# Optimization experiments

Measured on AMD Instinct MI355X. Metric: run time of the kernel, lower is better.

## Reference

```python
import jax, jax.numpy as jnp
import numpy as np
from functools import partial

# --- constants from module init / yolov5 NMS conventions ---
CONF_THRES = 0.25
IOU_THRES = 0.45
PATCH_CONF = 0.001
GN = jnp.array([640.0, 640.0, 640.0, 640.0])  # img_size[[1,0,1,0]]
MAX_WH = 4096.0       # per-class NMS offset trick
K_CLEAN = 256         # fixed-size cap for clean detections (max_det=1000 effectively)
K_PATCH = 1024        # fixed-size cap for patch detections (max_det=30000 effectively)
MAXDET_CLEAN = 1000
MAXDET_PATCH = 30000
B, N, NC = 8, 25200, 80


def xywh2xyxy(x):
    xy, wh = x[..., :2], x[..., 2:4]
    return jnp.concatenate([xy - wh * 0.5, xy + wh * 0.5], axis=-1)


def pairwise_iou(a, b):
    # a: [A,4], b: [B,4] -> [A,B] jaccard overlap (same math as IoU.get_iou)
    tl = jnp.maximum(a[:, None, :2], b[None, :, :2])
    br = jnp.minimum(a[:, None, 2:], b[None, :, 2:])
    wh = jnp.clip(br - tl, 0.0)
    inter = wh[..., 0] * wh[..., 1]
    area_a = (a[:, 2] - a[:, 0]) * (a[:, 3] - a[:, 1])
    area_b = (b[:, 2] - b[:, 0]) * (b[:, 3] - b[:, 1])
    return inter / (area_a[:, None] + area_b[None, :] - inter)


def greedy_nms(iou_mat, valid, iou_thres):
    # iou_mat: [K,K] (score-sorted order), valid: [K] bool. Greedy suppression.
    K = valid.shape[0]
    j = jnp.arange(K)

    def body(i, keep):
        suppress = keep[i] & (iou_mat[i] > iou_thres) & (j > i)
        return keep & ~suppress

    return jax.lax.fori_loop(0, K, body, valid)


def _nms_single(pred, conf_thres, K, max_det):
    # pred: [N, 5+nc] raw yolov5 prediction for one image
    boxes = xywh2xyxy(pred[:, :4])
    obj = pred[:, 4]
    cls_scores = pred[:, 5:] * obj[:, None]          # conf = obj * cls
    conf = cls_scores.max(axis=-1)
    cls = jnp.argmax(cls_scores, axis=-1).astype(pred.dtype)
    valid = (obj > conf_thres) & (conf > conf_thres)
    mscore = jnp.where(valid, conf, -1.0)
    _, idx = jax.lax.top_k(mscore, K)                # fixed-size candidate prefilter
    bk, ck, vk = boxes[idx], cls[idx], valid[idx]
    off_boxes = bk + (ck * MAX_WH)[:, None]          # class-offset NMS
    iou = pairwise_iou(off_boxes, off_boxes)
    keep = greedy_nms(jax.lax.stop_gradient(iou), vk, IOU_THRES)
    keep = keep & (jnp.cumsum(keep.astype(jnp.int32)) <= max_det)
    return bk, ck, keep


def _forward(output_clean, output_patch):
    nms_clean = jax.vmap(lambda p: _nms_single(p, CONF_THRES, K_CLEAN, MAXDET_CLEAN))
    nms_patch = jax.vmap(lambda p: _nms_single(p, PATCH_CONF, K_PATCH, MAXDET_PATCH))
    bc, cc, kc = nms_clean(output_clean)   # [B,Kc,4],[B,Kc],[B,Kc]
    bp, cp, kp = nms_patch(output_patch)   # [B,Kp,4],[B,Kp],[B,Kp]
    bc_n = bc / GN
    bp_n = bp / GN

    def per_img(bp_i, cp_i, kp_i, bc_i, cc_i, kc_i):
        iou = pairwise_iou(bp_i, bc_i)                       # [Kp, Kc]
        match = kp_i[:, None] & (cp_i[:, None] == cc_i[None, :])
        tm = jnp.max(jnp.where(match, iou, 0.0), axis=0)     # max IoU per clean det
        return jnp.sum(jnp.where(kc_i, tm, 0.0)), jnp.sum(kc_i.astype(jnp.float32))

    sums, counts = jax.vmap(per_img)(bp_n, cp, kp, bc_n, cc, kc)
    total, cnt = sums.sum(), counts.sum()
    return jnp.where(cnt > 0, 1.0 - total / jnp.maximum(cnt, 1.0), 1.0)


def setup_inputs() -> dict:
    key = jax.random.key(0)
    k1, k2 = jax.random.split(key)

    def make(k):
        kxy, kwh, ko, kc = jax.random.split(k, 4)
        xy = jax.random.uniform(kxy, (B, N, 2)) * 608.0 + 16.0   # centers in-frame
        wh = jax.random.uniform(kwh, (B, N, 2)) * 96.0 + 8.0     # plausible box sizes
        obj = jax.random.uniform(ko, (B, N, 1))
        cls = jax.random.uniform(kc, (B, N, NC))
        return jnp.concatenate([xy, wh, obj, cls], axis=-1)

    return {"output_clean": make(k1), "output_patch": make(k2)}


def reference(output_clean, output_patch):
    return _forward(output_clean, output_patch)
```

## Files before the change

kernel.cpp:

```cpp
#include <hip/hip_runtime.h>

#define N_ANCH 25200
#define NCLS   80
#define ROW    85
#define NIMG   16
#define KMAX   1024
#define NBINS  4096
#define CAND_CAP 4096
#define SC2_RPC 16
#define SC2_CPI 1575
#define SC2_CHUNKS (NIMG * SC2_CPI)
#define SC2_CFLOATS (SC2_RPC * ROW)
#define SC2_BLOCKS 1792
#define PCHUNK 64
#define CCNT_STRIDE 16

typedef unsigned long long u64;
typedef unsigned int u32;

#define OFF_KEYS 0ull
#define OFF_HIST 3225600ull
#define OFF_TBIN 3487744ull
#define OFF_CCNT 3487808ull
#define OFF_SUMS 3488832ull
#define OFF_CNTS 3488864ull
#define OFF_CAND 3488896ull
#define OFF_SEL  4013184ull
#define OFF_BOX  4144256ull
#define OFF_CLS  4406400ull
#define OFF_RINIT 4471936ull
#define OFF_KEEP 4473984ull
#define WS_NEED  4539520ull
#define ZERO_BYTES (262144ull + 64 + 1024 + 32 + 32)

#define DMA16(gsrc, ldst) \
    __builtin_amdgcn_global_load_lds( \
        (const __attribute__((address_space(1))) void*)(gsrc), \
        (__attribute__((address_space(3))) void*)(ldst), 16, 0, 0)

__device__ __forceinline__ int key_bin(u64 key) {
    u32 hi = (u32)(key >> 32);
    if (hi == 0u) return 0;
    float conf = __uint_as_float(hi - 0x40000000u);
    int b = 1 + (int)(conf * 4093.0f);
    return b > 4094 ? 4094 : b;
}

__device__ __forceinline__ u64 readlane64(u64 v, int src) {
    u32 lo = (u32)__builtin_amdgcn_readlane((int)(u32)(v & 0xffffffffull), src);
    u32 hi = (u32)__builtin_amdgcn_readlane((int)(u32)(v >> 32), src);
    return ((u64)hi << 32) | (u64)lo;
}

__device__ __forceinline__ u64 shfl64_xor(u64 v, int m) {
    int lo = __shfl_xor((int)(u32)(v & 0xffffffffull), m, 64);
    int hi = __shfl_xor((int)(u32)(v >> 32), m, 64);
    return ((u64)(u32)hi << 32) | (u64)(u32)lo;
}

__device__ __forceinline__ void sc_issue(const float* __restrict__ clean,
                                         const float* __restrict__ patch,
                                         int c, int lane, float* buf)
{
    const int b = c / SC2_CPI;
    const int ch = c - b * SC2_CPI;
    const float* g = ((b < 8) ? clean + (size_t)b * N_ANCH * ROW
                              : patch + (size_t)(b - 8) * N_ANCH * ROW)
                     + (size_t)ch * SC2_CFLOATS;
    #pragma unroll
    for (int u = 0; u < 5; ++u)
        DMA16(g + u * 256 + lane * 4, buf + u * 256);
    if (lane < 20)
        DMA16(g + 5 * 256 + lane * 4, buf + 5 * 256);
}

__device__ __forceinline__ void sc_compute(int c, int lane,
                                           const float* buf, u64* __restrict__ keys)
{
    const int b = c / SC2_CPI;
    const int ch = c - b * SC2_CPI;
    const int r = lane & 15, h = lane >> 4;
    const float* p = buf + r * ROW;
    const float obj = p[4];
    float best = -1.0f; int bc = 0;
    #pragma unroll
    for (int d = 0; d < 20; ++d) {
        const float s = p[5 + h * 20 + d] * obj;
        if (s > best) { best = s; bc = h * 20 + d; }
    }
    #pragma unroll
    for (int m = 16; m <= 32; m <<= 1) {
        const float o = __shfl_xor(best, m, 64);
        const int  oc = __shfl_xor(bc, m, 64);
        if (o > best || (o == best && oc < bc)) { best = o; bc = oc; }
    }
    if (h == 0) {
        const int n = ch * SC2_RPC + r;
        const float th = (b < 8) ? 0.25f : 0.001f;
        const bool valid = (obj > th) && (best > th);
        const u32 hi = valid ? (__float_as_uint(best) + 0x40000000u) : 0u;
        const u32 nbar = 32767u - (u32)n;
        keys[(size_t)b * N_ANCH + n] =
            ((u64)hi << 32) | ((u64)nbar << 8) | (u64)(u32)bc;
    }
}

__global__ __launch_bounds__(128) void k_score(const float* __restrict__ clean,
                                               const float* __restrict__ patch,
                                               u64* __restrict__ keys)
{
    __shared__ float lds[2][2][SC2_CFLOATS];
    const int wv = threadIdx.x >> 6, lane = threadIdx.x & 63;
    const int wid = blockIdx.x * 2 + wv;
    const int stride = SC2_BLOCKS * 2;
    int cur = 0;
    sc_issue(clean, patch, wid, lane, &lds[wv][0][0]);
    for (int c = wid; c < SC2_CHUNKS; c += stride) {
        const int cn = c + stride;
        if (cn < SC2_CHUNKS) {
            sc_issue(clean, patch, cn, lane, &lds[wv][cur ^ 1][0]);
            asm volatile("s_waitcnt vmcnt(6)" ::: "memory");
        } else {
            asm volatile("s_waitcnt vmcnt(0)" ::: "memory");
        }
        __builtin_amdgcn_sched_barrier(0);
        sc_compute(c, lane, &lds[wv][cur][0], keys);
        cur ^= 1;
    }
}

__global__ __launch_bounds__(256) void k_hist(const u64* __restrict__ keys,
                                              int* __restrict__ hist)
{
    __shared__ int h[NBINS];
    const int b = blockIdx.x;
    for (int i = threadIdx.x; i < NBINS; i += 256) h[i] = 0;
    __syncthreads();
    const int start = blockIdx.y * 1575;
    const u64* kp = keys + (size_t)b * N_ANCH;
    for (int i = start + threadIdx.x; i < start + 1575; i += 256)
        atomicAdd(&h[key_bin(kp[i])], 1);
    __syncthreads();
    for (int i = threadIdx.x; i < NBINS; i += 256)
        if (h[i]) atomicAdd(&hist[b * NBINS + i], h[i]);
}

__global__ __launch_bounds__(1024) void k_thresh(const int* __restrict__ hist,
                                                 int* __restrict__ tbin)
{
    __shared__ int arr[1024];
    const int b = blockIdx.x;
    const int t = threadIdx.x;
    int hh[4];
    hh[0] = hist[b * NBINS + 4 * t + 0];
    hh[1] = hist[b * NBINS + 4 * t + 1];
    hh[2] = hist[b * NBINS + 4 * t + 2];
    hh[3] = hist[b * NBINS + 4 * t + 3];
    const int r = hh[0] + hh[1] + hh[2] + hh[3];
    arr[t] = r;
    __syncthreads();
    for (int off = 1; off < 1024; off <<= 1) {
        int v = (t + off < 1024) ? arr[t + off] : 0;
        __syncthreads();
        arr[t] += v;
        __syncthreads();
    }
    const int K = (b < 8) ? 256 : 1024;
    int cb = arr[t] - r;
    for (int d = 3; d >= 0; --d) {
        int ca = cb + hh[d];
        if (cb < K && ca >= K) tbin[b] = 4 * t + d;
        cb = ca;
    }
}

__global__ __launch_bounds__(256) void k_compact(const u64* __restrict__ keys,
                                                 const int* __restrict__ tbin,
                                                 int* __restrict__ ccnt,
                                                 u64* __restrict__ cand)
{
    const int b = blockIdx.x;
    const int T = tbin[b];
    const u64* kp = keys + (size_t)b * N_ANCH;
    const int start = blockIdx.y * 1575;
    const int lane = threadIdx.x & 63;
    #pragma unroll
    for (int it = 0; it < 7; ++it) {
        const int off = it * 256 + threadIdx.x;
        const bool in = off < 1575;
        const u64 key = in ? kp[start + off] : 0ull;
        const bool cnd = in && (key_bin(key) >= T);
        const u64 bal = __ballot(cnd);
        if (bal) {
            int base = 0;
            if (lane == 0) base = atomicAdd(&ccnt[b * CCNT_STRIDE], __popcll(bal));
            base = __shfl(base, 0, 64);
            if (cnd) {
                const int pos = base + __popcll(bal & ((1ull << lane) - 1ull));
                if (pos < CAND_CAP) cand[(size_t)b * CAND_CAP + pos] = key;
            }
        }
    }
}

__global__ __launch_bounds__(1024) void k_sort(const u64* __restrict__ cand,
                                               const int* __restrict__ ccnt,
                                               u64* __restrict__ sel)
{
    __shared__ u64 sk[CAND_CAP];
    const int b = blockIdx.x;
    const int C = min(ccnt[b * CCNT_STRIDE], CAND_CAP);
    const int t = threadIdx.x;
    u64 e0, e1, e2, e3;
    e0 = (t < C) ? cand[(size_t)b * CAND_CAP + t] : 0ull;
    e1 = (1024 + t < C) ? cand[(size_t)b * CAND_CAP + 1024 + t] : 0ull;
    e2 = (2048 + t < C) ? cand[(size_t)b * CAND_CAP + 2048 + t] : 0ull;
    e3 = (3072 + t < C) ? cand[(size_t)b * CAND_CAP + 3072 + t] : 0ull;

    #define CSWAP_D(a, c) { if ((a) < (c)) { u64 _t = (a); (a) = (c); (c) = _t; } }
    #define CSWAP_A(a, c) { if ((a) > (c)) { u64 _t = (a); (a) = (c); (c) = _t; } }

    for (int k = 2; k <= 4096; k <<= 1) {
        for (int j = k >> 1; j > 0; j >>= 1) {
            if (j >= 1024) {
                if (j == 2048) {
                    CSWAP_D(e0, e2); CSWAP_D(e1, e3);
                } else {
                    if (k == 4096) { CSWAP_D(e0, e1); CSWAP_D(e2, e3); }
                    else           { CSWAP_D(e0, e1); CSWAP_A(e2, e3); }
                }
            } else if (j >= 64) {
                __syncthreads();
                sk[t] = e0; sk[1024 + t] = e1; sk[2048 + t] = e2; sk[3072 + t] = e3;
                __syncthreads();
                const int tp = t ^ j;
                #pragma unroll
                for (int p = 0; p < 4; ++p) {
                    const int i = p * 1024 + t;
                    const u64 cv = (p == 0) ? e0 : (p == 1) ? e1 : (p == 2) ? e2 : e3;
                    const u64 o = sk[p * 1024 + tp];
                    const bool take_max = (((i & k) == 0) == ((t & j) == 0));
                    const u64 mx = cv > o ? cv : o;
                    const u64 mn = cv > o ? o : cv;
                    const u64 nv = take_max ? mx : mn;
                    if (p == 0) e0 = nv; else if (p == 1) e1 = nv;
                    else if (p == 2) e2 = nv; else e3 = nv;
                }
            } else {
                #pragma unroll
                for (int p = 0; p < 4; ++p) {
                    const int i = p * 1024 + t;
                    const u64 cv = (p == 0) ? e0 : (p == 1) ? e1 : (p == 2) ? e2 : e3;
                    const u64 o = shfl64_xor(cv, j);
                    const bool take_max = (((i & k) == 0) == ((t & j) == 0));
                    const u64 mx = cv > o ? cv : o;
                    const u64 mn = cv > o ? o : cv;
                    const u64 nv = take_max ? mx : mn;
                    if (p == 0) e0 = nv; else if (p == 1) e1 = nv;
                    else if (p == 2) e2 = nv; else e3 = nv;
                }
            }
        }
    }
    const int K = (b < 8) ? 256 : 1024;
    if (t < K) sel[b * KMAX + t] = e0;
    #undef CSWAP_D
    #undef CSWAP_A
}

__global__ __launch_bounds__(1024) void k_gather(const float* __restrict__ clean,
                                                 const float* __restrict__ patch,
                                                 const u64* __restrict__ sel,
                                                 float4* __restrict__ boxes,
                                                 int* __restrict__ cls,
                                                 u64* __restrict__ rinit)
{
    const int b = blockIdx.x;
    const int t = threadIdx.x;
    const int K = (b < 8) ? 256 : 1024;
    const u64 key = (t < K) ? sel[b * KMAX + t] : 0ull;
    const u32 hi = (u32)(key >> 32);
    const bool valid = (t < K) && (hi != 0u);
    u64 bal = __ballot(valid);
    if ((t & 63) == 0) rinit[b * 16 + (t >> 6)] = ~bal;
    if (t >= K) return;
    const int n = 32767 - (int)((key >> 8) & 0x7FFFu);
    const int c = (int)(key & 0x7Fu);
    const float* src = ((b < 8) ? (clean + (size_t)b * N_ANCH * ROW)
                                : (patch + (size_t)(b - 8) * N_ANCH * ROW)) + (size_t)n * ROW;
    const float x = src[0], y = src[1], w = src[2], h = src[3];
    boxes[b * KMAX + t] = make_float4(x - w * 0.5f, y - h * 0.5f, x + w * 0.5f, y + h * 0.5f);
    cls[b * KMAX + t] = c;
}

__global__ __launch_bounds__(1024) void k_nms_mask(const float4* __restrict__ boxes,
                                                   const int* __restrict__ cls,
                                                   u64* __restrict__ mask,
                                                   u64* __restrict__ diag)
{
    __shared__ float4 bx[KMAX];
    __shared__ float ar[KMAX];
    const int b = blockIdx.x;
    const int K = (b < 8) ? 256 : 1024;
    const int row0 = blockIdx.y * 64;
    if (row0 >= K) return;
    const int t = threadIdx.x;
    for (int i = t; i < K; i += 1024) {
        float4 v = boxes[b * KMAX + i];
        float off = (float)cls[b * KMAX + i] * 4096.0f;
        v.x += off; v.y += off; v.z += off; v.w += off;
        bx[i] = v;
        ar[i] = (v.z - v.x) * (v.w - v.y);
    }
    __syncthreads();
    const int w   = t >> 6;
    const int row = row0 + (t & 63);
    u64* dst = mask + ((size_t)b * KMAX + row) * 16 + w;
    if (((w << 6) + 63) <= row0 && row0 > 0) { *dst = 0ull; return; }
    const float4 bi = bx[row];
    const float ai = ar[row];
    const int jbase = w << 6;
    u64 m = 0;
    #pragma unroll 8
    for (int k = 0; k < 64; ++k) {
        const int j = jbase + k;
        const float4 bj = bx[j];
        const float ax = fmaxf(bi.x, bj.x), ay = fmaxf(bi.y, bj.y);
        const float bx2 = fminf(bi.z, bj.z), by2 = fminf(bi.w, bj.w);
        const float iw = fmaxf(bx2 - ax, 0.f), ih = fmaxf(by2 - ay, 0.f);
        const float inter = iw * ih;
        const float iou = inter / (ai + ar[j] - inter);
        if (j > row && iou > 0.45f) m |= (1ull << k);
    }
    *dst = m;
    if (w == (row0 >> 6)) diag[(size_t)b * KMAX + row] = m;
}

__global__ __launch_bounds__(1024) void k_nms_scan(const u64* __restrict__ mask,
                                                   const u64* __restrict__ diag,
                                                   const u64* __restrict__ rinit,
                                                   int* __restrict__ keep)
{
    extern __shared__ u64 smem[];
    const int b = blockIdx.x;
    const int K = (b < 8) ? 256 : 1024;
    const int W = K >> 6;
    const int t = threadIdx.x;
    u64* smask = smem;
    u64* sdiag = smem + (size_t)K * 16;
    {
        const float4* s4 = (const float4*)(mask + (size_t)b * KMAX * 16);
        float4* d4 = (float4*)smask;
        const int n4 = (K * 16) >> 1;
        for (int i = t; i < n4; i += 1024) d4[i] = s4[i];
        const float4* s4d = (const float4*)(diag + (size_t)b * KMAX);
        float4* d4d = (float4*)sdiag;
        for (int i = t; i < (K >> 1); i += 1024) d4d[i] = s4d[i];
    }
    __syncthreads();
    if (t >= 64) return;
    const int lane = t;
    const int q = lane >> 4;
    const int wl = lane & 15;
    u64 w_remv = rinit[b * 16 + wl];
    u64 ow = readlane64(w_remv, 0);
    u64 dj = sdiag[lane];
    for (int g = 0; g < W; ++g) {
        u64 nz = __ballot(dj != 0ull);
        u64 o = ow;
        while (nz) {
            const int j = (int)__builtin_ctzll(nz);
            nz &= nz - 1;
            if (!((o >> j) & 1ull)) o |= readlane64(dj, j);
        }
        const u64 kept = ~o;
        if (g + 1 < W) dj = sdiag[(g + 1) * 64 + lane];
        const u64* mrow = smask + (size_t)(g * 64 + q * 16) * 16 + wl;
        const u32 kg = (u32)((kept >> (q * 16)) & 0xFFFFull);
        u64 a0 = 0, a1 = 0;
        #pragma unroll
        for (int i = 0; i < 16; i += 2) {
            const u64 m0 = mrow[(size_t)(i + 0) * 16];
            const u64 m1 = mrow[(size_t)(i + 1) * 16];
            a0 |= ((kg >> i) & 1u) ? m0 : 0ull;
            a1 |= ((kg >> (i + 1)) & 1u) ? m1 : 0ull;
        }
        u64 part = a0 | a1;
        part |= shfl64_xor(part, 16);
        part |= shfl64_xor(part, 32);
        w_remv |= part;
        if (g + 1 < W) ow = readlane64(w_remv, g + 1);
    }
    if (lane < W) {
        #pragma unroll
        for (int k = 0; k < 64; ++k)
            keep[b * KMAX + lane * 64 + k] = (int)(((w_remv >> k) & 1) ^ 1ull);
    }
}

__global__ __launch_bounds__(256) void k_match_partial(const float4* __restrict__ boxes,
                                                       const int* __restrict__ cls,
                                                       const int* __restrict__ keep,
                                                       float* __restrict__ pmax)
{
    __shared__ float4 pb[PCHUNK];
    __shared__ float par[PCHUNK];
    __shared__ int pcls[PCHUNK];
    const int c = blockIdx.x;
    const int p = blockIdx.y;
    const int bp = 8 + c;
    const int t = threadIdx.x;
    if (t < PCHUNK) {
        const int i = p * PCHUNK + t;
        const float4 v = boxes[bp * KMAX + i];
        pb[t] = v;
        par[t] = (v.z - v.x) * (v.w - v.y);
        pcls[t] = keep[bp * KMAX + i] ? cls[bp * KMAX + i] : -1;
    }
    __syncthreads();
    const float4 bc = boxes[c * KMAX + t];
    const int cc = cls[c * KMAX + t];
    const float area_c = (bc.z - bc.x) * (bc.w - bc.y);
    float tm = 0.f;
    #pragma unroll 8
    for (int i = 0; i < PCHUNK; ++i) {
        const float4 bi = pb[i];
        const float ax = fmaxf(bi.x, bc.x), ay = fmaxf(bi.y, bc.y);
        const float bx2 = fminf(bi.z, bc.z), by2 = fminf(bi.w, bc.w);
        const float iw = fmaxf(bx2 - ax, 0.f), ih = fmaxf(by2 - ay, 0.f);
        const float inter = iw * ih;
        const float iou = inter / (par[i] + area_c - inter);
        tm = fmaxf(tm, (pcls[i] == cc) ? iou : 0.f);
    }
    pmax[(c * 16 + p) * 256 + t] = tm;
}

__global__ __launch_bounds__(256) void k_match_reduce(const float* __restrict__ pmax,
                                                      const int* __restrict__ keep,
                                                      float* __restrict__ sums,
                                                      float* __restrict__ cnts)
{
    __shared__ float red[8];
    const int c = blockIdx.x;
    const int t = threadIdx.x;
    float tm = 0.f;
    #pragma unroll
    for (int p = 0; p < 16; ++p)
        tm = fmaxf(tm, pmax[(c * 16 + p) * 256 + t]);
    const int kc = keep[c * KMAX + t];
    float val = kc ? tm : 0.f;
    float cv  = kc ? 1.f : 0.f;
    for (int off = 32; off > 0; off >>= 1) {
        val += __shfl_down(val, off);
        cv  += __shfl_down(cv, off);
    }
    const int wv = t >> 6, lane = t & 63;
    if (lane == 0) { red[wv] = val; red[4 + wv] = cv; }
    __syncthreads();
    if (t == 0) {
        sums[c] = red[0] + red[1] + red[2] + red[3];
        cnts[c] = red[4] + red[5] + red[6] + red[7];
    }
}

__global__ void k_final(const float* __restrict__ sums,
                        const float* __restrict__ cnts,
                        float* __restrict__ out)
{
    if (threadIdx.x == 0 && blockIdx.x == 0) {
        float total = 0.f, cnt = 0.f;
        for (int c = 0; c < 8; ++c) { total += sums[c]; cnt += cnts[c]; }
        out[0] = (cnt > 0.f) ? (1.0f - total / fmaxf(cnt, 1.0f)) : 1.0f;
    }
}

extern "C" void kernel_launch(void* const* d_in, const int* in_sizes, int n_in,
                              void* d_out, int out_size, void* d_ws, size_t ws_size,
                              hipStream_t stream)
{
    if (ws_size < WS_NEED) return;
    const float* clean = (const float*)d_in[0];
    const float* patch = (const float*)d_in[1];
    float* out = (float*)d_out;
    char* ws = (char*)d_ws;

    u64*    keys = (u64*)(ws + OFF_KEYS);
    u64*    mask = (u64*)(ws + OFF_KEYS);
    int*    hist = (int*)(ws + OFF_HIST);
    u64*    diag = (u64*)(ws + OFF_HIST);
    int*    tbin = (int*)(ws + OFF_TBIN);
    int*    ccnt = (int*)(ws + OFF_CCNT);
    float*  sums = (float*)(ws + OFF_SUMS);
    float*  cnts = (float*)(ws + OFF_CNTS);
    u64*    cand = (u64*)(ws + OFF_CAND);
    float*  pmax = (float*)(ws + OFF_CAND);
    u64*    sel  = (u64*)(ws + OFF_SEL);
    float4* boxes = (float4*)(ws + OFF_BOX);
    int*    cls  = (int*)(ws + OFF_CLS);
    u64*    rinit = (u64*)(ws + OFF_RINIT);
    int*    keep = (int*)(ws + OFF_KEEP);

    hipMemsetAsync(ws + OFF_HIST, 0, ZERO_BYTES, stream);

    k_score<<<SC2_BLOCKS, 128, 0, stream>>>(clean, patch, keys);
    k_hist<<<dim3(NIMG, 16), 256, 0, stream>>>(keys, hist);
    k_thresh<<<NIMG, 1024, 0, stream>>>(hist, tbin);
    k_compact<<<dim3(NIMG, 16), 256, 0, stream>>>(keys, tbin, ccnt, cand);
    k_sort<<<NIMG, 1024, 0, stream>>>(cand, ccnt, sel);
    k_gather<<<NIMG, 1024, 0, stream>>>(clean, patch, sel, boxes, cls, rinit);
    k_nms_mask<<<dim3(NIMG, 16), 1024, 0, stream>>>(boxes, cls, mask, diag);
    k_nms_scan<<<NIMG, 1024, KMAX * 16 * 8 + KMAX * 8, stream>>>(mask, diag, rinit, keep);
    k_match_partial<<<dim3(8, 16), 256, 0, stream>>>(boxes, cls, keep, pmax);
    k_match_reduce<<<8, 256, 0, stream>>>(pmax, keep, sums, cnts);
    k_final<<<1, 64, 0, stream>>>(sums, cnts, out);
}
```

Baseline: 136.1 us.

## Fuse histogram into scoring, gather into NMS mask, and final reductions

```diff
diff --git a/kernel.cpp b/kernel.cpp
--- a/kernel.cpp
+++ b/kernel.cpp
@@ -5,13 +5,13 @@
 #define ROW    85
 #define NIMG   16
 #define KMAX   1024
-#define NBINS  4096
+#define NBINS  1024
 #define CAND_CAP 4096
 #define SC2_RPC 16
 #define SC2_CPI 1575
-#define SC2_CHUNKS (NIMG * SC2_CPI)
-#define SC2_CFLOATS (SC2_RPC * ROW)
-#define SC2_BLOCKS 1792
+#define SC2_CFLOATS (SC2_RPC*ROW)
+#define SC2_BPI 96
+#define SC2_WPI 192
 #define PCHUNK 64
 #define CCNT_STRIDE 16
 
@@ -20,18 +20,16 @@
 
 #define OFF_KEYS 0ull
 #define OFF_HIST 3225600ull
-#define OFF_TBIN 3487744ull
-#define OFF_CCNT 3487808ull
-#define OFF_SUMS 3488832ull
-#define OFF_CNTS 3488864ull
-#define OFF_CAND 3488896ull
-#define OFF_SEL  4013184ull
-#define OFF_BOX  4144256ull
-#define OFF_CLS  4406400ull
-#define OFF_RINIT 4471936ull
-#define OFF_KEEP 4473984ull
-#define WS_NEED  4539520ull
-#define ZERO_BYTES (262144ull + 64 + 1024 + 32 + 32)
+#define OFF_TBIN 3291136ull
+#define OFF_CCNT 3291200ull
+#define OFF_CAND 3292224ull
+#define OFF_SEL  3816512ull
+#define OFF_BOX  3947584ull
+#define OFF_CLS  4209728ull
+#define OFF_RINIT 4275264ull
+#define OFF_KEEP 4277312ull
+#define WS_NEED  4342848ull
+#define ZERO_BYTES 66624ull
 
 #define DMA16(gsrc, ldst) \
     __builtin_amdgcn_global_load_lds( \
@@ -42,8 +40,8 @@
     u32 hi = (u32)(key >> 32);
     if (hi == 0u) return 0;
     float conf = __uint_as_float(hi - 0x40000000u);
-    int b = 1 + (int)(conf * 4093.0f);
-    return b > 4094 ? 4094 : b;
+    int b = 1 + (int)(conf * 1022.0f);
+    return b > 1023 ? 1023 : b;
 }
 
 __device__ __forceinline__ u64 readlane64(u64 v, int src) {
@@ -58,27 +56,20 @@
     return ((u64)(u32)hi << 32) | (u64)(u32)lo;
 }
 
-__device__ __forceinline__ void sc_issue(const float* __restrict__ clean,
-                                         const float* __restrict__ patch,
-                                         int c, int lane, float* buf)
-{
-    const int b = c / SC2_CPI;
-    const int ch = c - b * SC2_CPI;
-    const float* g = ((b < 8) ? clean + (size_t)b * N_ANCH * ROW
-                              : patch + (size_t)(b - 8) * N_ANCH * ROW)
-                     + (size_t)ch * SC2_CFLOATS;
+__device__ __forceinline__ void sc_issue(const float* __restrict__ img, int ch,
+                                         int lane, float* buf)
+{
+    const float* s = img + (size_t)ch * SC2_CFLOATS;
     #pragma unroll
     for (int u = 0; u < 5; ++u)
-        DMA16(g + u * 256 + lane * 4, buf + u * 256);
+        DMA16(s + u * 256 + lane * 4, buf + u * 256);
     if (lane < 20)
-        DMA16(g + 5 * 256 + lane * 4, buf + 5 * 256);
-}
-
-__device__ __forceinline__ void sc_compute(int c, int lane,
-                                           const float* buf, u64* __restrict__ keys)
-{
-    const int b = c / SC2_CPI;
-    const int ch = c - b * SC2_CPI;
+        DMA16(s + 1280 + lane * 4, buf + 1280);
+}
+
+__device__ __forceinline__ void sc_compute(int b, int c, int lane, const float* buf,
+                                           u64* __restrict__ keys, int* bh)
+{
     const int r = lane & 15, h = lane >> 4;
     const float* p = buf + r * ROW;
     const float obj = p[4];
@@ -95,10 +86,15 @@
         if (o > best || (o == best && oc < bc)) { best = o; bc = oc; }
     }
     if (h == 0) {
-        const int n = ch * SC2_RPC + r;
+        const int n = c * SC2_RPC + r;
         const float th = (b < 8) ? 0.25f : 0.001f;
         const bool valid = (obj > th) && (best > th);
         const u32 hi = valid ? (__float_as_uint(best) + 0x40000000u) : 0u;
+        if (valid) {
+            int bin = 1 + (int)(best * 1022.0f);
+            if (bin > 1023) bin = 1023;
+            atomicAdd(&bh[bin], 1);
+        }
         const u32 nbar = 32767u - (u32)n;
         keys[(size_t)b * N_ANCH + n] =
             ((u64)hi << 32) | ((u64)nbar << 8) | (u64)(u32)bc;
@@ -107,48 +103,43 @@
 
 __global__ __launch_bounds__(128) void k_score(const float* __restrict__ clean,
                                                const float* __restrict__ patch,
-                                               u64* __restrict__ keys)
+                                               u64* __restrict__ keys,
+                                               int* __restrict__ hist)
 {
     __shared__ float lds[2][2][SC2_CFLOATS];
-    const int wv = threadIdx.x >> 6, lane = threadIdx.x & 63;
-    const int wid = blockIdx.x * 2 + wv;
-    const int stride = SC2_BLOCKS * 2;
+    __shared__ int bh[NBINS];
+    const int t = threadIdx.x;
+    const int wv = t >> 6, lane = t & 63;
+    const int b = blockIdx.x / SC2_BPI;
+    const int blk = blockIdx.x - b * SC2_BPI;
+    const int wimg = blk * 2 + wv;
+    for (int i = t; i < NBINS; i += 128) bh[i] = 0;
+    __syncthreads();
+    const float* img = (b < 8) ? clean + (size_t)b * N_ANCH * ROW
+                               : patch + (size_t)(b - 8) * N_ANCH * ROW;
     int cur = 0;
-    sc_issue(clean, patch, wid, lane, &lds[wv][0][0]);
-    for (int c = wid; c < SC2_CHUNKS; c += stride) {
-        const int cn = c + stride;
-        if (cn < SC2_CHUNKS) {
-            sc_issue(clean, patch, cn, lane, &lds[wv][cur ^ 1][0]);
+    sc_issue(img, wimg, lane, &lds[wv][0][0]);
+    for (int c = wimg; c < SC2_CPI; c += SC2_WPI) {
+        const int cn = c + SC2_WPI;
+        if (cn < SC2_CPI) {
+            sc_issue(img, cn, lane, &lds[wv][cur ^ 1][0]);
             asm volatile("s_waitcnt vmcnt(6)" ::: "memory");
         } else {
             asm volatile("s_waitcnt vmcnt(0)" ::: "memory");
         }
         __builtin_amdgcn_sched_barrier(0);
-        sc_compute(c, lane, &lds[wv][cur][0], keys);
+        sc_compute(b, c, lane, &lds[wv][cur][0], keys, bh);
         cur ^= 1;
     }
-}
-
-__global__ __launch_bounds__(256) void k_hist(const u64* __restrict__ keys,
-                                              int* __restrict__ hist)
-{
-    __shared__ int h[NBINS];
-    const int b = blockIdx.x;
-    for (int i = threadIdx.x; i < NBINS; i += 256) h[i] = 0;
-    __syncthreads();
-    const int start = blockIdx.y * 1575;
-    const u64* kp = keys + (size_t)b * N_ANCH;
-    for (int i = start + threadIdx.x; i < start + 1575; i += 256)
-        atomicAdd(&h[key_bin(kp[i])], 1);
-    __syncthreads();
-    for (int i = threadIdx.x; i < NBINS; i += 256)
-        if (h[i]) atomicAdd(&hist[b * NBINS + i], h[i]);
-}
-
-__global__ __launch_bounds__(1024) void k_thresh(const int* __restrict__ hist,
-                                                 int* __restrict__ tbin)
-{
-    __shared__ int arr[1024];
+    __syncthreads();
+    for (int i = t; i < NBINS; i += 128)
+        if (bh[i]) atomicAdd(&hist[b * NBINS + i], bh[i]);
+}
+
+__global__ __launch_bounds__(256) void k_thresh(const int* __restrict__ hist,
+                                                int* __restrict__ tbin)
+{
+    __shared__ int arr[256];
     const int b = blockIdx.x;
     const int t = threadIdx.x;
     int hh[4];
@@ -159,8 +150,8 @@
     const int r = hh[0] + hh[1] + hh[2] + hh[3];
     arr[t] = r;
     __syncthreads();
-    for (int off = 1; off < 1024; off <<= 1) {
-        int v = (t + off < 1024) ? arr[t + off] : 0;
+    for (int off = 1; off < 256; off <<= 1) {
+        int v = (t + off < 256) ? arr[t + off] : 0;
         __syncthreads();
         arr[t] += v;
         __syncthreads();
@@ -216,16 +207,13 @@
     e1 = (1024 + t < C) ? cand[(size_t)b * CAND_CAP + 1024 + t] : 0ull;
     e2 = (2048 + t < C) ? cand[(size_t)b * CAND_CAP + 2048 + t] : 0ull;
     e3 = (3072 + t < C) ? cand[(size_t)b * CAND_CAP + 3072 + t] : 0ull;
-
     #define CSWAP_D(a, c) { if ((a) < (c)) { u64 _t = (a); (a) = (c); (c) = _t; } }
     #define CSWAP_A(a, c) { if ((a) > (c)) { u64 _t = (a); (a) = (c); (c) = _t; } }
-
     for (int k = 2; k <= 4096; k <<= 1) {
         for (int j = k >> 1; j > 0; j >>= 1) {
             if (j >= 1024) {
-                if (j == 2048) {
-                    CSWAP_D(e0, e2); CSWAP_D(e1, e3);
-                } else {
+                if (j == 2048) { CSWAP_D(e0, e2); CSWAP_D(e1, e3); }
+                else {
                     if (k == 4096) { CSWAP_D(e0, e1); CSWAP_D(e2, e3); }
                     else           { CSWAP_D(e0, e1); CSWAP_A(e2, e3); }
                 }
@@ -268,49 +256,44 @@
     #undef CSWAP_A
 }
 
-__global__ __launch_bounds__(1024) void k_gather(const float* __restrict__ clean,
-                                                 const float* __restrict__ patch,
-                                                 const u64* __restrict__ sel,
-                                                 float4* __restrict__ boxes,
-                                                 int* __restrict__ cls,
-                                                 u64* __restrict__ rinit)
-{
-    const int b = blockIdx.x;
-    const int t = threadIdx.x;
-    const int K = (b < 8) ? 256 : 1024;
-    const u64 key = (t < K) ? sel[b * KMAX + t] : 0ull;
-    const u32 hi = (u32)(key >> 32);
-    const bool valid = (t < K) && (hi != 0u);
-    u64 bal = __ballot(valid);
-    if ((t & 63) == 0) rinit[b * 16 + (t >> 6)] = ~bal;
-    if (t >= K) return;
-    const int n = 32767 - (int)((key >> 8) & 0x7FFFu);
-    const int c = (int)(key & 0x7Fu);
-    const float* src = ((b < 8) ? (clean + (size_t)b * N_ANCH * ROW)
-                                : (patch + (size_t)(b - 8) * N_ANCH * ROW)) + (size_t)n * ROW;
-    const float x = src[0], y = src[1], w = src[2], h = src[3];
-    boxes[b * KMAX + t] = make_float4(x - w * 0.5f, y - h * 0.5f, x + w * 0.5f, y + h * 0.5f);
-    cls[b * KMAX + t] = c;
-}
-
-__global__ __launch_bounds__(1024) void k_nms_mask(const float4* __restrict__ boxes,
-                                                   const int* __restrict__ cls,
+__global__ __launch_bounds__(1024) void k_nms_mask(const float* __restrict__ clean,
+                                                   const float* __restrict__ patch,
+                                                   const u64* __restrict__ sel,
+                                                   float4* __restrict__ boxes,
+                                                   int* __restrict__ cls,
+                                                   u64* __restrict__ rinit,
                                                    u64* __restrict__ mask,
                                                    u64* __restrict__ diag)
 {
     __shared__ float4 bx[KMAX];
     __shared__ float ar[KMAX];
-    const int b = blockIdx.x;
+    const int b = blockIdx.x, y = blockIdx.y;
     const int K = (b < 8) ? 256 : 1024;
-    const int row0 = blockIdx.y * 64;
+    const int row0 = y * 64;
     if (row0 >= K) return;
     const int t = threadIdx.x;
-    for (int i = t; i < K; i += 1024) {
-        float4 v = boxes[b * KMAX + i];
-        float off = (float)cls[b * KMAX + i] * 4096.0f;
-        v.x += off; v.y += off; v.z += off; v.w += off;
-        bx[i] = v;
-        ar[i] = (v.z - v.x) * (v.w - v.y);
+    {
+        const u64 key = (t < K) ? sel[b * KMAX + t] : 0ull;
+        const u32 hi = (u32)(key >> 32);
+        const bool valid = (t < K) && (hi != 0u);
+        const u64 bal = __ballot(valid);
+        if (y == 0 && (t & 63) == 0) rinit[b * 16 + (t >> 6)] = ~bal;
+        if (t < K) {
+            const int n = 32767 - (int)((key >> 8) & 0x7FFFu);
+            const int c = (int)(key & 0x7Fu);
+            const float* src = ((b < 8) ? (clean + (size_t)b * N_ANCH * ROW)
+                                        : (patch + (size_t)(b - 8) * N_ANCH * ROW))
+                               + (size_t)n * ROW;
+            const float x = src[0], yy = src[1], w = src[2], h = src[3];
+            const float4 raw = make_float4(x - w * 0.5f, yy - h * 0.5f,
+                                           x + w * 0.5f, yy + h * 0.5f);
+            if (y == 0) { boxes[b * KMAX + t] = raw; cls[b * KMAX + t] = c; }
+            const float off = (float)c * 4096.0f;
+            const float4 ob = make_float4(raw.x + off, raw.y + off,
+                                          raw.z + off, raw.w + off);
+            bx[t] = ob;
+            ar[t] = (ob.z - ob.x) * (ob.w - ob.y);
+        }
     }
     __syncthreads();
     const int w   = t >> 6;
@@ -435,43 +418,36 @@
     pmax[(c * 16 + p) * 256 + t] = tm;
 }
 
-__global__ __launch_bounds__(256) void k_match_reduce(const float* __restrict__ pmax,
-                                                      const int* __restrict__ keep,
-                                                      float* __restrict__ sums,
-                                                      float* __restrict__ cnts)
+__global__ __launch_bounds__(256) void k_match_final(const float* __restrict__ pmax,
+                                                     const int* __restrict__ keep,
+                                                     float* __restrict__ out)
 {
     __shared__ float red[8];
-    const int c = blockIdx.x;
-    const int t = threadIdx.x;
-    float tm = 0.f;
-    #pragma unroll
-    for (int p = 0; p < 16; ++p)
-        tm = fmaxf(tm, pmax[(c * 16 + p) * 256 + t]);
-    const int kc = keep[c * KMAX + t];
-    float val = kc ? tm : 0.f;
-    float cv  = kc ? 1.f : 0.f;
-    for (int off = 32; off > 0; off >>= 1) {
-        val += __shfl_down(val, off);
-        cv  += __shfl_down(cv, off);
-    }
-    const int wv = t >> 6, lane = t & 63;
-    if (lane == 0) { red[wv] = val; red[4 + wv] = cv; }
-    __syncthreads();
-    if (t == 0) {
-        sums[c] = red[0] + red[1] + red[2] + red[3];
-        cnts[c] = red[4] + red[5] + red[6] + red[7];
-    }
-}
-
-__global__ void k_final(const float* __restrict__ sums,
-                        const float* __restrict__ cnts,
-                        float* __restrict__ out)
-{
-    if (threadIdx.x == 0 && blockIdx.x == 0) {
-        float total = 0.f, cnt = 0.f;
-        for (int c = 0; c < 8; ++c) { total += sums[c]; cnt += cnts[c]; }
-        out[0] = (cnt > 0.f) ? (1.0f - total / fmaxf(cnt, 1.0f)) : 1.0f;
-    }
+    const int t = threadIdx.x;
+    float tot = 0.f, cn = 0.f;
+    for (int c = 0; c < 8; ++c) {
+        float tm = 0.f;
+        #pragma unroll
+        for (int p = 0; p < 16; ++p)
+            tm = fmaxf(tm, pmax[(c * 16 + p) * 256 + t]);
+        const int kc = keep[c * KMAX + t];
+        float val = kc ? tm : 0.f;
+        float cv  = kc ? 1.f : 0.f;
+        for (int off = 32; off > 0; off >>= 1) {
+            val += __shfl_down(val, off);
+            cv  += __shfl_down(cv, off);
+        }
+        const int wv = t >> 6, lane = t & 63;
+        if (lane == 0) { red[wv] = val; red[4 + wv] = cv; }
+        __syncthreads();
+        if (t == 0) {
+            tot += red[0] + red[1] + red[2] + red[3];
+            cn  += red[4] + red[5] + red[6] + red[7];
+        }
+        __syncthreads();
+    }
+    if (t == 0)
+        out[0] = (cn > 0.f) ? (1.0f - tot / fmaxf(cn, 1.0f)) : 1.0f;
 }
 
 extern "C" void kernel_launch(void* const* d_in, const int* in_sizes, int n_in,
@@ -487,12 +463,10 @@
     u64*    keys = (u64*)(ws + OFF_KEYS);
     u64*    mask = (u64*)(ws + OFF_KEYS);
     int*    hist = (int*)(ws + OFF_HIST);
-    u64*    diag = (u64*)(ws + OFF_HIST);
     int*    tbin = (int*)(ws + OFF_TBIN);
     int*    ccnt = (int*)(ws + OFF_CCNT);
-    float*  sums = (float*)(ws + OFF_SUMS);
-    float*  cnts = (float*)(ws + OFF_CNTS);
     u64*    cand = (u64*)(ws + OFF_CAND);
+    u64*    diag = (u64*)(ws + OFF_CAND);
     float*  pmax = (float*)(ws + OFF_CAND);
     u64*    sel  = (u64*)(ws + OFF_SEL);
     float4* boxes = (float4*)(ws + OFF_BOX);
@@ -502,15 +476,13 @@
 
     hipMemsetAsync(ws + OFF_HIST, 0, ZERO_BYTES, stream);
 
-    k_score<<<SC2_BLOCKS, 128, 0, stream>>>(clean, patch, keys);
-    k_hist<<<dim3(NIMG, 16), 256, 0, stream>>>(keys, hist);
-    k_thresh<<<NIMG, 1024, 0, stream>>>(hist, tbin);
+    k_score<<<NIMG * SC2_BPI, 128, 0, stream>>>(clean, patch, keys, hist);
+    k_thresh<<<NIMG, 256, 0, stream>>>(hist, tbin);
     k_compact<<<dim3(NIMG, 16), 256, 0, stream>>>(keys, tbin, ccnt, cand);
     k_sort<<<NIMG, 1024, 0, stream>>>(cand, ccnt, sel);
-    k_gather<<<NIMG, 1024, 0, stream>>>(clean, patch, sel, boxes, cls, rinit);
-    k_nms_mask<<<dim3(NIMG, 16), 1024, 0, stream>>>(boxes, cls, mask, diag);
+    k_nms_mask<<<dim3(NIMG, 16), 1024, 0, stream>>>(clean, patch, sel, boxes, cls,
+                                                    rinit, mask, diag);
     k_nms_scan<<<NIMG, 1024, KMAX * 16 * 8 + KMAX * 8, stream>>>(mask, diag, rinit, keep);
     k_match_partial<<<dim3(8, 16), 256, 0, stream>>>(boxes, cls, keep, pmax);
-    k_match_reduce<<<8, 256, 0, stream>>>(pmax, keep, sums, cnts);
-    k_final<<<1, 64, 0, stream>>>(sums, cnts, out);
-}
+    k_match_final<<<1, 256, 0, stream>>>(pmax, keep, out);
+}
```

New measurement: 133.6 us. Within noise of the previous version (-1.8%).
